# Kernel tuning notes

Hardware: AMD Instinct MI355X
Metric: run time of the kernel (lower is better)

The kernel has to match this reference:

```python
import jax, jax.numpy as jnp
import numpy as np

NUM_USERS = 600000
NUM_ITEMS = 400000
NUM_NODES = NUM_USERS + NUM_ITEMS
DIM = 64
NUM_EDGES = 8000000


def setup_inputs() -> dict:
    key = jax.random.key(0)
    k1, k2, k3, k4 = jax.random.split(key, 4)
    users_emb = jax.random.normal(k1, (NUM_USERS, DIM), dtype=jnp.float32)
    items_emb = jax.random.normal(k2, (NUM_ITEMS, DIM), dtype=jnp.float32)
    edge_index = jax.random.randint(k3, (2, NUM_EDGES), 0, NUM_NODES, dtype=jnp.int64)
    edge_values = jax.random.uniform(k4, (NUM_EDGES,), dtype=jnp.float32)
    return {
        "users_emb": users_emb,
        "items_emb": items_emb,
        "edge_index": edge_index,
        "edge_values": edge_values,
    }


def reference(users_emb, items_emb, edge_index, edge_values):
    # all_emb = cat([users_emb, items_emb])  -> [N, d]
    num_user = users_emb.shape[0]
    num_item = items_emb.shape[0]
    all_emb = jnp.concatenate([users_emb, items_emb], axis=0)
    # SpMM: out[r] = sum_{e: row[e]==r} val[e] * all_emb[col[e]]
    rows, cols = edge_index[0], edge_index[1]
    messages = all_emb[cols] * edge_values[:, None]  # [E, d] gather + scale
    out = jax.ops.segment_sum(messages, rows, num_segments=num_user + num_item)
    h_u2 = out[:num_user]
    h_i2 = out[num_user:]
    return (h_u2, h_i2)
```

## Files before the change

### kernel.cpp

```cpp
#include <hip/hip_runtime.h>

#define DIM 64
#define RPB 1024
#define RPB_SHIFT 10
#define NBMAX 1024
#define CHUNK 4096
#define EPT 16
#define CAPT 36
#define NPG 4
#define NPB 128
#define REC_CAP 1536

typedef unsigned long long u64;
typedef unsigned int u32;
typedef unsigned short u16;
typedef float f4v __attribute__((ext_vector_type(4)));
typedef _Float16 h4 __attribute__((ext_vector_type(4)));
typedef _Float16 h8 __attribute__((ext_vector_type(8)));

__global__ void detect_idx_width(const unsigned int* __restrict__ idx_words,
                                 int* __restrict__ flag) {
    __shared__ unsigned int s_or[256];
    unsigned int acc = 0;
    for (int i = threadIdx.x; i < 4096; i += blockDim.x)
        acc |= idx_words[2 * i + 1];
    s_or[threadIdx.x] = acc;
    __syncthreads();
    for (int s = 128; s > 0; s >>= 1) {
        if (threadIdx.x < s) s_or[threadIdx.x] |= s_or[threadIdx.x + s];
        __syncthreads();
    }
    if (threadIdx.x == 0) *flag = (s_or[0] == 0) ? 1 : 0;
}

__device__ __forceinline__ int load_idx(const void* ei, int use64, long long i) {
    return use64 ? (int)((const long long*)ei)[i] : ((const int*)ei)[i];
}

__global__ __launch_bounds__(256) void convert_emb(const f4v* __restrict__ u4,
                                                   const f4v* __restrict__ i4,
                                                   long long usz4, long long tot4,
                                                   h4* __restrict__ dst) {
    long long stride = (long long)gridDim.x * blockDim.x;
    for (long long idx = (long long)blockIdx.x * blockDim.x + threadIdx.x;
         idx < tot4; idx += stride) {
        const f4v* src = (idx < usz4) ? (u4 + idx) : (i4 + (idx - usz4));
        f4v f = __builtin_nontemporal_load(src);
        h4 o;
        o.x = (_Float16)f.x; o.y = (_Float16)f.y;
        o.z = (_Float16)f.z; o.w = (_Float16)f.w;
        __builtin_nontemporal_store(o, dst + idx);
    }
}

__global__ __launch_bounds__(256) void hist_coarse(const void* __restrict__ ei,
                                                   const int* __restrict__ flag,
                                                   int* __restrict__ counts,
                                                   int num_edges) {
    __shared__ int h[NBMAX];
    for (int b = threadIdx.x; b < NBMAX; b += 256) h[b] = 0;
    __syncthreads();
    int use64 = *flag;
    long long tid = (long long)blockIdx.x * 256 + threadIdx.x;
    long long stride = (long long)gridDim.x * 256;
    long long npairs = (long long)num_edges >> 1;
    if (use64) {
        const ulonglong2* p = (const ulonglong2*)ei;
        for (long long e = tid; e < npairs; e += stride) {
            ulonglong2 rr = p[e];
            atomicAdd(&h[(int)(u32)rr.x >> RPB_SHIFT], 1);
            atomicAdd(&h[(int)(u32)rr.y >> RPB_SHIFT], 1);
        }
    } else {
        const int2* p = (const int2*)ei;
        for (long long e = tid; e < npairs; e += stride) {
            int2 rr = p[e];
            atomicAdd(&h[rr.x >> RPB_SHIFT], 1);
            atomicAdd(&h[rr.y >> RPB_SHIFT], 1);
        }
    }
    if (tid == 0 && (num_edges & 1)) {
        int r = load_idx(ei, use64, num_edges - 1);
        atomicAdd(&h[r >> RPB_SHIFT], 1);
    }
    __syncthreads();
    for (int b = threadIdx.x; b < NBMAX; b += 256)
        if (h[b]) atomicAdd(&counts[b], h[b]);
}

__global__ __launch_bounds__(256) void scan_buckets(const int* __restrict__ counts,
                                                    int* __restrict__ offs,
                                                    int* __restrict__ gcursor,
                                                    int* __restrict__ offs2, int nbkt) {
    __shared__ int ps[256];
    int t = threadIdx.x;
    int4 h = ((const int4*)counts)[t];
    ps[t] = h.x + h.y + h.z + h.w;
    __syncthreads();
    for (int st = 1; st < 256; st <<= 1) {
        int add = (t >= st) ? ps[t - st] : 0;
        __syncthreads();
        ps[t] += add;
        __syncthreads();
    }
    int ep = (t > 0) ? ps[t - 1] : 0;
    int o0 = ep, o1 = o0 + h.x, o2 = o1 + h.y, o3 = o2 + h.z;
    offs[4*t] = o0; offs[4*t+1] = o1; offs[4*t+2] = o2; offs[4*t+3] = o3;
    gcursor[4*t] = o0; gcursor[4*t+1] = o1; gcursor[4*t+2] = o2; gcursor[4*t+3] = o3;
    if (t == 255) {
        offs[NBMAX] = ps[255];
        offs2[(long long)nbkt << RPB_SHIFT] = ps[255];
    }
}

__global__ __launch_bounds__(256) void bin_edges(const void* __restrict__ ei,
                                                 const float* __restrict__ vals,
                                                 const int* __restrict__ flag,
                                                 int* __restrict__ gcursor,
                                                 u64* __restrict__ recs,
                                                 int num_edges) {
    __shared__ u32 hist[NBMAX];
    __shared__ u32 scanL[NBMAX];
    __shared__ u32 gbase[NBMAX];
    __shared__ u32 ps[256];
    __shared__ u64 payload[CHUNK];
    __shared__ u16 bidv[CHUNK];

    int tid = threadIdx.x;
    long long base = (long long)blockIdx.x * CHUNK;
    int n = (int)min((long long)CHUNK, (long long)num_edges - base);
    int use64 = *flag;

    for (int b = tid; b < NBMAX; b += 256) hist[b] = 0;
    __syncthreads();

    int rows_[EPT]; int cols_[EPT]; float ws_[EPT];
    #pragma unroll
    for (int i = 0; i < EPT; ++i) {
        int j = tid + i * 256;
        rows_[i] = -1;
        if (j < n) {
            long long e = base + j;
            rows_[i] = load_idx(ei, use64, e);
            cols_[i] = load_idx(ei, use64, (long long)num_edges + e);
            ws_[i]   = vals[e];
            atomicAdd(&hist[rows_[i] >> RPB_SHIFT], 1u);
        }
    }
    __syncthreads();

    u32 h0 = hist[4*tid], h1 = hist[4*tid+1], h2 = hist[4*tid+2], h3 = hist[4*tid+3];
    ps[tid] = h0 + h1 + h2 + h3;
    __syncthreads();
    for (int st = 1; st < 256; st <<= 1) {
        u32 add = (tid >= st) ? ps[tid - st] : 0;
        __syncthreads();
        ps[tid] += add;
        __syncthreads();
    }
    u32 ep = (tid > 0) ? ps[tid - 1] : 0;
    scanL[4*tid]   = ep;
    scanL[4*tid+1] = ep + h0;
    scanL[4*tid+2] = ep + h0 + h1;
    scanL[4*tid+3] = ep + h0 + h1 + h2;
    __syncthreads();

    for (int b = tid; b < NBMAX; b += 256) {
        u32 c = hist[b];
        gbase[b] = c ? (u32)atomicAdd(&gcursor[b], (int)c) : 0u;
    }
    __syncthreads();
    for (int b = tid; b < NBMAX; b += 256) hist[b] = scanL[b];
    __syncthreads();

    #pragma unroll
    for (int i = 0; i < EPT; ++i) {
        if (rows_[i] >= 0) {
            int b = rows_[i] >> RPB_SHIFT;
            u32 pos = atomicAdd(&hist[b], 1u);
            u32 rl = (u32)(rows_[i] & (RPB - 1));
            payload[pos] = ((u64)__float_as_uint(ws_[i]) << 32) | (rl << 20) | (u32)cols_[i];
            bidv[pos] = (u16)b;
        }
    }
    __syncthreads();

    for (int j = tid; j < n; j += 256) {
        u64 rec = payload[j];
        int b = bidv[j];
        recs[gbase[b] + (u32)j - scanL[b]] = rec;
    }
}

__global__ __launch_bounds__(256, 2) void sort_bucket(const int* __restrict__ offs,
                                                      u64* __restrict__ recs,
                                                      int* __restrict__ offs2) {
    __shared__ u32 bins[RPB];
    __shared__ u32 ps[256];
    int b = blockIdx.x;
    int t = threadIdx.x;
    int beg = offs[b], end = offs[b + 1];
    int cnt = end - beg;
    int row0 = b << RPB_SHIFT;

    if (cnt > CAPT * 256) {
        for (int i = t; i < RPB; i += 256) offs2[row0 + i] = -(b + 1);
        return;
    }

    u64 r_[CAPT];
    #pragma unroll
    for (int k = 0; k < CAPT; ++k) {
        int j = t + k * 256;
        r_[k] = (j < cnt) ? recs[beg + j] : 0ull;
    }
    for (int i = t; i < RPB; i += 256) bins[i] = 0;
    __syncthreads();

    #pragma unroll
    for (int k = 0; k < CAPT; ++k) {
        int j = t + k * 256;
        if (j < cnt) atomicAdd(&bins[(u32)(r_[k] >> 20) & (RPB - 1)], 1u);
    }
    __syncthreads();

    u32 c0[4]; u32 s = 0;
    #pragma unroll
    for (int i = 0; i < 4; ++i) { c0[i] = bins[t * 4 + i]; s += c0[i]; }
    ps[t] = s;
    __syncthreads();
    for (int st = 1; st < 256; st <<= 1) {
        u32 add = (t >= st) ? ps[t - st] : 0;
        __syncthreads();
        ps[t] += add;
        __syncthreads();
    }
    u32 ex = (t > 0) ? ps[t - 1] : 0;
    #pragma unroll
    for (int i = 0; i < 4; ++i) {
        bins[t * 4 + i] = ex;
        offs2[row0 + t * 4 + i] = beg + (int)ex;
        ex += c0[i];
    }
    __syncthreads();

    #pragma unroll
    for (int k = 0; k < CAPT; ++k) {
        int j = t + k * 256;
        if (j < cnt) {
            u32 rl = (u32)(r_[k] >> 20) & (RPB - 1);
            u32 pos = atomicAdd(&bins[rl], 1u);
            recs[beg + pos] = r_[k];
        }
    }
}

#define ACC8(P0, P1, W, V) \
    P0.x += W * (float)V[0]; P0.y += W * (float)V[1]; \
    P0.z += W * (float)V[2]; P0.w += W * (float)V[3]; \
    P1.x += W * (float)V[4]; P1.y += W * (float)V[5]; \
    P1.z += W * (float)V[6]; P1.w += W * (float)V[7];

__global__ __launch_bounds__(256) void gather_nodes_h(const int* __restrict__ offs,
                                                      const int* __restrict__ offs2,
                                                      const u64* __restrict__ recs,
                                                      const h8* __restrict__ hemb8,
                                                      float* __restrict__ out,
                                                      int num_nodes) {
    __shared__ int s_offs[NPB + 1];
    __shared__ int s_bad;
    __shared__ u64 s_recs[REC_CAP];

    int tid = threadIdx.x;
    int l8  = tid & 7;
    int g   = tid >> 3;
    long long n0 = (long long)blockIdx.x * NPB;

    if (tid == 0) s_bad = 0;
    __syncthreads();
    if (tid <= NPB) {
        int v = offs2[n0 + tid];
        s_offs[tid] = v;
        if (v < 0) s_bad = 1;
    }
    __syncthreads();

    int rbeg = s_offs[0];
    int cnt  = s_offs[NPB] - rbeg;
    bool fast = (s_bad == 0) && ((u32)cnt <= (u32)REC_CAP);

    if (fast) {
        for (int j = tid; j < cnt; j += 256)
            s_recs[j] = __builtin_nontemporal_load(&recs[rbeg + j]);
    }
    __syncthreads();

    if (fast) {
        for (int nn = 0; nn < NPG; ++nn) {
            int ln = g * NPG + nn;
            int node = (int)n0 + ln;
            if (node >= num_nodes) break;
            int beg = s_offs[ln] - rbeg;
            int end = s_offs[ln + 1] - rbeg;

            float4 p0 = make_float4(0.f,0.f,0.f,0.f), p1 = make_float4(0.f,0.f,0.f,0.f);
            float4 q0 = make_float4(0.f,0.f,0.f,0.f), q1 = make_float4(0.f,0.f,0.f,0.f);

            int i = beg;
            for (; i + 8 <= end; i += 8) {
                u64 s0 = s_recs[i];     u64 s1 = s_recs[i + 1];
                u64 s2 = s_recs[i + 2]; u64 s3 = s_recs[i + 3];
                u64 s4 = s_recs[i + 4]; u64 s5 = s_recs[i + 5];
                u64 s6 = s_recs[i + 6]; u64 s7 = s_recs[i + 7];
                h8 v0 = hemb8[(((u32)s0 & 0xFFFFFu) << 3) + l8];
                h8 v1 = hemb8[(((u32)s1 & 0xFFFFFu) << 3) + l8];
                h8 v2 = hemb8[(((u32)s2 & 0xFFFFFu) << 3) + l8];
                h8 v3 = hemb8[(((u32)s3 & 0xFFFFFu) << 3) + l8];
                h8 v4 = hemb8[(((u32)s4 & 0xFFFFFu) << 3) + l8];
                h8 v5 = hemb8[(((u32)s5 & 0xFFFFFu) << 3) + l8];
                h8 v6 = hemb8[(((u32)s6 & 0xFFFFFu) << 3) + l8];
                h8 v7 = hemb8[(((u32)s7 & 0xFFFFFu) << 3) + l8];
                float w0 = __uint_as_float((u32)(s0 >> 32));
                float w1 = __uint_as_float((u32)(s1 >> 32));
                float w2 = __uint_as_float((u32)(s2 >> 32));
                float w3 = __uint_as_float((u32)(s3 >> 32));
                float w4 = __uint_as_float((u32)(s4 >> 32));
                float w5 = __uint_as_float((u32)(s5 >> 32));
                float w6 = __uint_as_float((u32)(s6 >> 32));
                float w7 = __uint_as_float((u32)(s7 >> 32));
                ACC8(p0, p1, w0, v0); ACC8(q0, q1, w1, v1);
                ACC8(p0, p1, w2, v2); ACC8(q0, q1, w3, v3);
                ACC8(p0, p1, w4, v4); ACC8(q0, q1, w5, v5);
                ACC8(p0, p1, w6, v6); ACC8(q0, q1, w7, v7);
            }
            if (i < end) {
                int last = end - 1;
                int e1 = min(i + 1, last), e2 = min(i + 2, last);
                int e3 = min(i + 3, last), e4 = min(i + 4, last);
                int e5 = min(i + 5, last), e6 = min(i + 6, last);
                u64 s0 = s_recs[i];  u64 s1 = s_recs[e1];
                u64 s2 = s_recs[e2]; u64 s3 = s_recs[e3];
                u64 s4 = s_recs[e4]; u64 s5 = s_recs[e5];
                u64 s6 = s_recs[e6];
                h8 v0 = hemb8[(((u32)s0 & 0xFFFFFu) << 3) + l8];
                h8 v1 = hemb8[(((u32)s1 & 0xFFFFFu) << 3) + l8];
                h8 v2 = hemb8[(((u32)s2 & 0xFFFFFu) << 3) + l8];
                h8 v3 = hemb8[(((u32)s3 & 0xFFFFFu) << 3) + l8];
                h8 v4 = hemb8[(((u32)s4 & 0xFFFFFu) << 3) + l8];
                h8 v5 = hemb8[(((u32)s5 & 0xFFFFFu) << 3) + l8];
                h8 v6 = hemb8[(((u32)s6 & 0xFFFFFu) << 3) + l8];
                float w0 = __uint_as_float((u32)(s0 >> 32));
                float w1 = (i + 1 < end) ? __uint_as_float((u32)(s1 >> 32)) : 0.f;
                float w2 = (i + 2 < end) ? __uint_as_float((u32)(s2 >> 32)) : 0.f;
                float w3 = (i + 3 < end) ? __uint_as_float((u32)(s3 >> 32)) : 0.f;
                float w4 = (i + 4 < end) ? __uint_as_float((u32)(s4 >> 32)) : 0.f;
                float w5 = (i + 5 < end) ? __uint_as_float((u32)(s5 >> 32)) : 0.f;
                float w6 = (i + 6 < end) ? __uint_as_float((u32)(s6 >> 32)) : 0.f;
                ACC8(p0, p1, w0, v0); ACC8(q0, q1, w1, v1);
                ACC8(p0, p1, w2, v2); ACC8(q0, q1, w3, v3);
                ACC8(p0, p1, w4, v4); ACC8(q0, q1, w5, v5);
                ACC8(p0, p1, w6, v6);
            }

            p0.x += q0.x; p0.y += q0.y; p0.z += q0.z; p0.w += q0.w;
            p1.x += q1.x; p1.y += q1.y; p1.z += q1.z; p1.w += q1.w;
            f4v o0; o0.x = p0.x; o0.y = p0.y; o0.z = p0.z; o0.w = p0.w;
            f4v o1; o1.x = p1.x; o1.y = p1.y; o1.z = p1.z; o1.w = p1.w;
            f4v* dst = (f4v*)out + ((long long)node << 4) + (l8 << 1);
            __builtin_nontemporal_store(o0, dst);
            __builtin_nontemporal_store(o1, dst + 1);
        }
    } else {
        for (int nn = 0; nn < NPG; ++nn) {
            int ln = g * NPG + nn;
            int node = (int)n0 + ln;
            if (node >= num_nodes) break;
            int beg = s_offs[ln];
            int end = s_offs[ln + 1];
            if (beg < 0) { int b = node >> RPB_SHIFT; beg = offs[b]; end = offs[b + 1]; }
            else if (end < 0) { end = offs[(node >> RPB_SHIFT) + 1]; }
            u32 rl = (u32)(node & (RPB - 1));

            float4 p0 = make_float4(0.f,0.f,0.f,0.f), p1 = make_float4(0.f,0.f,0.f,0.f);
            float4 q0 = make_float4(0.f,0.f,0.f,0.f), q1 = make_float4(0.f,0.f,0.f,0.f);
            int last = end - 1;
            u32 rm = RPB - 1;
            for (int i = beg; i < end; i += 4) {
                int e1 = min(i + 1, last), e2 = min(i + 2, last), e3 = min(i + 3, last);
                u64 s0 = recs[i];  u64 s1 = recs[e1];
                u64 s2 = recs[e2]; u64 s3 = recs[e3];
                h8 v0 = hemb8[(((u32)s0 & 0xFFFFFu) << 3) + l8];
                h8 v1 = hemb8[(((u32)s1 & 0xFFFFFu) << 3) + l8];
                h8 v2 = hemb8[(((u32)s2 & 0xFFFFFu) << 3) + l8];
                h8 v3 = hemb8[(((u32)s3 & 0xFFFFFu) << 3) + l8];
                float w0 = ((((u32)(s0 >> 20)) & rm) == rl)
                           ? __uint_as_float((u32)(s0 >> 32)) : 0.f;
                float w1 = (((((u32)(s1 >> 20)) & rm) == rl) & (i + 1 < end))
                           ? __uint_as_float((u32)(s1 >> 32)) : 0.f;
                float w2 = (((((u32)(s2 >> 20)) & rm) == rl) & (i + 2 < end))
                           ? __uint_as_float((u32)(s2 >> 32)) : 0.f;
                float w3 = (((((u32)(s3 >> 20)) & rm) == rl) & (i + 3 < end))
                           ? __uint_as_float((u32)(s3 >> 32)) : 0.f;
                ACC8(p0, p1, w0, v0); ACC8(q0, q1, w1, v1);
                ACC8(p0, p1, w2, v2); ACC8(q0, q1, w3, v3);
            }
            p0.x += q0.x; p0.y += q0.y; p0.z += q0.z; p0.w += q0.w;
            p1.x += q1.x; p1.y += q1.y; p1.z += q1.z; p1.w += q1.w;
            f4v o0; o0.x = p0.x; o0.y = p0.y; o0.z = p0.z; o0.w = p0.w;
            f4v o1; o1.x = p1.x; o1.y = p1.y; o1.z = p1.z; o1.w = p1.w;
            f4v* dst = (f4v*)out + ((long long)node << 4) + (l8 << 1);
            __builtin_nontemporal_store(o0, dst);
            __builtin_nontemporal_store(o1, dst + 1);
        }
    }
}

__device__ __forceinline__ void gstep(u64 s, u32 rl,
                                      const float* __restrict__ users,
                                      const float* __restrict__ items_m,
                                      int num_users, int l16, float4& a) {
    int c = (int)(s & 0xFFFFFu);
    float w = __uint_as_float((u32)(s >> 32));
    w = (((u32)(s >> 20) & (RPB - 1)) == rl) ? w : 0.f;
    const float* p = ((c < num_users) ? users : items_m) + ((u32)c << 6);
    float4 m = reinterpret_cast<const float4*>(p)[l16];
    a.x += w * m.x; a.y += w * m.y; a.z += w * m.z; a.w += w * m.w;
}

__global__ __launch_bounds__(256) void gather_nodes(const int* __restrict__ offs,
                                                    const int* __restrict__ offs2,
                                                    const u64* __restrict__ recs,
                                                    const float* __restrict__ users,
                                                    const float* __restrict__ items_m,
                                                    float* __restrict__ out,
                                                    int num_users, int num_nodes) {
    int node = blockIdx.x * (blockDim.x >> 6) + (threadIdx.x >> 6);
    int lane = threadIdx.x & 63;
    if (node >= num_nodes) return;
    int q   = lane >> 4;
    int l16 = lane & 15;

    int beg = offs2[node];
    int end = offs2[node + 1];
    if (beg < 0) { int b = node >> RPB_SHIFT; beg = offs[b]; end = offs[b + 1]; }
    else if (end < 0) { end = offs[(node >> RPB_SHIFT) + 1]; }
    u32 rl = (u32)(node & (RPB - 1));

    float4 a0 = make_float4(0.f, 0.f, 0.f, 0.f);
    float4 a1 = make_float4(0.f, 0.f, 0.f, 0.f);

    int i = beg + q;
    for (; i + 4 < end; i += 8) {
        u64 s0 = recs[i];
        u64 s1 = recs[i + 4];
        gstep(s0, rl, users, items_m, num_users, l16, a0);
        gstep(s1, rl, users, items_m, num_users, l16, a1);
    }
    if (i < end) {
        u64 s0 = recs[i];
        gstep(s0, rl, users, items_m, num_users, l16, a0);
    }
    a0.x += a1.x; a0.y += a1.y; a0.z += a1.z; a0.w += a1.w;

    for (int msk = 16; msk <= 32; msk <<= 1) {
        a0.x += __shfl_xor(a0.x, msk, 64);
        a0.y += __shfl_xor(a0.y, msk, 64);
        a0.z += __shfl_xor(a0.z, msk, 64);
        a0.w += __shfl_xor(a0.w, msk, 64);
    }
    if (q == 0)
        reinterpret_cast<float4*>(out)[(long long)node * 16 + l16] = a0;
}

__global__ __launch_bounds__(256) void scatter_edges(const void* __restrict__ edge_index,
                                                     const float* __restrict__ vals,
                                                     const float* __restrict__ users,
                                                     const float* __restrict__ items,
                                                     float* __restrict__ out,
                                                     const int* __restrict__ idx64_flag,
                                                     int num_users, int num_edges) {
    long long gid = (long long)blockIdx.x * blockDim.x + threadIdx.x;
    long long e = gid >> 4;
    int lane = (int)(gid & 15);
    if (e >= num_edges) return;
    int use64 = *idx64_flag;
    int r = load_idx(edge_index, use64, e);
    int c = load_idx(edge_index, use64, (long long)num_edges + e);
    float w = vals[e];
    const float* src = (c < num_users)
        ? (users + (long long)c * DIM)
        : (items + (long long)(c - num_users) * DIM);
    float4 m = reinterpret_cast<const float4*>(src)[lane];
    float* dst = out + (long long)r * DIM + lane * 4;
    unsafeAtomicAdd(dst + 0, m.x * w);
    unsafeAtomicAdd(dst + 1, m.y * w);
    unsafeAtomicAdd(dst + 2, m.z * w);
    unsafeAtomicAdd(dst + 3, m.w * w);
}

extern "C" void kernel_launch(void* const* d_in, const int* in_sizes, int n_in,
                              void* d_out, int out_size, void* d_ws, size_t ws_size,
                              hipStream_t stream) {
    const float* users = (const float*)d_in[0];
    const float* items = (const float*)d_in[1];
    const void*  eidx  = d_in[2];
    const float* vals  = (const float*)d_in[3];
    float* out = (float*)d_out;

    int num_users = in_sizes[0] / DIM;
    int num_items = in_sizes[1] / DIM;
    int num_nodes = num_users + num_items;
    int num_edges = in_sizes[3];
    int nbkt = (num_nodes + RPB - 1) >> RPB_SHIFT;

    size_t off = 0;
    auto alloc = [&](size_t bytes) { size_t p = off; off = (off + bytes + 255) & ~(size_t)255; return p; };
    size_t o_flag   = alloc(4);
    size_t o_counts = alloc((size_t)NBMAX * 4);
    size_t o_offs   = alloc(((size_t)NBMAX + 1) * 4);
    size_t o_gcur   = alloc((size_t)NBMAX * 4);
    size_t o_recs   = alloc((size_t)num_edges * 8 + 64);
    size_t o_offs2  = alloc((((size_t)nbkt << RPB_SHIFT) + 1) * 4);
    size_t need_base = off;
    size_t o_hemb   = alloc((size_t)num_nodes * DIM * 2);
    size_t need_f16 = off;

    char* ws = (char*)d_ws;
    int* flag = (int*)(ws + o_flag);

    detect_idx_width<<<1, 256, 0, stream>>>((const unsigned int*)eidx, flag);

    if (ws_size < need_base || nbkt > NBMAX || num_nodes > (1 << 20)) {
        hipMemsetAsync(d_out, 0, (size_t)out_size * sizeof(float), stream);
        long long total_threads = (long long)num_edges * 16;
        long long grid = (total_threads + 255) / 256;
        scatter_edges<<<(int)grid, 256, 0, stream>>>(
            eidx, vals, users, items, out, flag, num_users, num_edges);
        return;
    }

    int* counts  = (int*)(ws + o_counts);
    int* offs    = (int*)(ws + o_offs);
    int* gcursor = (int*)(ws + o_gcur);
    u64* recs    = (u64*)(ws + o_recs);
    int* offs2   = (int*)(ws + o_offs2);
    h4*  hemb4   = (h4*)(ws + o_hemb);

    bool use_f16 = (ws_size >= need_f16) && ((DIM % 8) == 0);

    hipMemsetAsync(counts, 0, (size_t)NBMAX * 4, stream);

    if (use_f16) {
        long long usz4 = (long long)num_users * DIM / 4;
        long long tot4 = (long long)num_nodes * DIM / 4;
        convert_emb<<<2048, 256, 0, stream>>>((const f4v*)users, (const f4v*)items,
                                              usz4, tot4, hemb4);
    }

    hist_coarse<<<1024, 256, 0, stream>>>(eidx, flag, counts, num_edges);
    scan_buckets<<<1, 256, 0, stream>>>(counts, offs, gcursor, offs2, nbkt);

    int bin_grid = (num_edges + CHUNK - 1) / CHUNK;
    bin_edges<<<bin_grid, 256, 0, stream>>>(eidx, vals, flag, gcursor, recs, num_edges);

    sort_bucket<<<nbkt, 256, 0, stream>>>(offs, recs, offs2);

    if (use_f16) {
        int gg = (num_nodes + NPB - 1) / NPB;
        gather_nodes_h<<<gg, 256, 0, stream>>>(offs, offs2, recs,
                                               (const h8*)hemb4, out, num_nodes);
    } else {
        int gg = (num_nodes + 3) / 4;
        const float* items_m = items - (size_t)num_users * DIM;
        gather_nodes<<<gg, 256, 0, stream>>>(offs, offs2, recs, users, items_m, out,
                                             num_users, num_nodes);
    }
}
```

Before: 466.5 us.

## Use wave-shuffle block scans, nontemporal index loads, larger binning chunks

Replaces the shared-memory Hillis-Steele block scans in scan_buckets, bin_edges and sort_bucket with a wave-level shuffle scan plus a small cross-wave combine, which removes many barriers. Raises the binning chunk to 6144 edges and 24 per thread with launch bounds of two blocks per CU, and shrinks the hist_coarse grid. Index and value loads become nontemporal, and the fp16 embedding store becomes a normal store so it can stay in cache for the gather. The larger chunk raises register and LDS use in bin_edges, which may cut occupancy.

```diff
diff --git a/kernel.cpp b/kernel.cpp
--- a/kernel.cpp
+++ b/kernel.cpp
@@ -4,8 +4,8 @@
 #define RPB 1024
 #define RPB_SHIFT 10
 #define NBMAX 1024
-#define CHUNK 4096
-#define EPT 16
+#define CHUNK 6144
+#define EPT 24
 #define CAPT 36
 #define NPG 4
 #define NPB 128
@@ -35,6 +35,28 @@
 
 __device__ __forceinline__ int load_idx(const void* ei, int use64, long long i) {
     return use64 ? (int)((const long long*)ei)[i] : ((const int*)ei)[i];
+}
+
+__device__ __forceinline__ int load_idx_nt(const void* ei, int use64, long long i) {
+    return use64 ? (int)__builtin_nontemporal_load(&((const long long*)ei)[i])
+                 : __builtin_nontemporal_load(&((const int*)ei)[i]);
+}
+
+__device__ __forceinline__ u32 quad_scan_ex(u32 qs, u32* wtot, int tid, u32* total_out) {
+    u32 inc = qs;
+    #pragma unroll
+    for (int d = 1; d < 64; d <<= 1) {
+        u32 v = __shfl_up(inc, d, 64);
+        if ((tid & 63) >= d) inc += v;
+    }
+    if ((tid & 63) == 63) wtot[tid >> 6] = inc;
+    __syncthreads();
+    int w = tid >> 6;
+    u32 woff = 0;
+    #pragma unroll
+    for (int k = 0; k < 3; ++k) woff += (k < w) ? wtot[k] : 0;
+    if (total_out) *total_out = wtot[0] + wtot[1] + wtot[2] + wtot[3];
+    return woff + inc - qs;
 }
 
 __global__ __launch_bounds__(256) void convert_emb(const f4v* __restrict__ u4,
@@ -49,7 +71,7 @@
         h4 o;
         o.x = (_Float16)f.x; o.y = (_Float16)f.y;
         o.z = (_Float16)f.z; o.w = (_Float16)f.w;
-        __builtin_nontemporal_store(o, dst + idx);
+        dst[idx] = o;
     }
 }
 
@@ -64,19 +86,19 @@
     long long tid = (long long)blockIdx.x * 256 + threadIdx.x;
     long long stride = (long long)gridDim.x * 256;
     long long npairs = (long long)num_edges >> 1;
+    const u64* p = (const u64*)ei;
     if (use64) {
-        const ulonglong2* p = (const ulonglong2*)ei;
         for (long long e = tid; e < npairs; e += stride) {
-            ulonglong2 rr = p[e];
-            atomicAdd(&h[(int)(u32)rr.x >> RPB_SHIFT], 1);
-            atomicAdd(&h[(int)(u32)rr.y >> RPB_SHIFT], 1);
+            u64 a = __builtin_nontemporal_load(&p[2 * e]);
+            u64 b = __builtin_nontemporal_load(&p[2 * e + 1]);
+            atomicAdd(&h[(int)(u32)a >> RPB_SHIFT], 1);
+            atomicAdd(&h[(int)(u32)b >> RPB_SHIFT], 1);
         }
     } else {
-        const int2* p = (const int2*)ei;
         for (long long e = tid; e < npairs; e += stride) {
-            int2 rr = p[e];
-            atomicAdd(&h[rr.x >> RPB_SHIFT], 1);
-            atomicAdd(&h[rr.y >> RPB_SHIFT], 1);
+            u64 v = __builtin_nontemporal_load(&p[e]);
+            atomicAdd(&h[(int)(u32)v >> RPB_SHIFT], 1);
+            atomicAdd(&h[(int)(u32)(v >> 32) >> RPB_SHIFT], 1);
         }
     }
     if (tid == 0 && (num_edges & 1)) {
@@ -92,37 +114,31 @@
                                                     int* __restrict__ offs,
                                                     int* __restrict__ gcursor,
                                                     int* __restrict__ offs2, int nbkt) {
-    __shared__ int ps[256];
+    __shared__ u32 wtot[4];
     int t = threadIdx.x;
     int4 h = ((const int4*)counts)[t];
-    ps[t] = h.x + h.y + h.z + h.w;
-    __syncthreads();
-    for (int st = 1; st < 256; st <<= 1) {
-        int add = (t >= st) ? ps[t - st] : 0;
-        __syncthreads();
-        ps[t] += add;
-        __syncthreads();
-    }
-    int ep = (t > 0) ? ps[t - 1] : 0;
-    int o0 = ep, o1 = o0 + h.x, o2 = o1 + h.y, o3 = o2 + h.z;
+    u32 qs = (u32)(h.x + h.y + h.z + h.w);
+    u32 total;
+    u32 ex = quad_scan_ex(qs, wtot, t, &total);
+    int o0 = (int)ex, o1 = o0 + h.x, o2 = o1 + h.y, o3 = o2 + h.z;
     offs[4*t] = o0; offs[4*t+1] = o1; offs[4*t+2] = o2; offs[4*t+3] = o3;
     gcursor[4*t] = o0; gcursor[4*t+1] = o1; gcursor[4*t+2] = o2; gcursor[4*t+3] = o3;
     if (t == 255) {
-        offs[NBMAX] = ps[255];
-        offs2[(long long)nbkt << RPB_SHIFT] = ps[255];
-    }
-}
-
-__global__ __launch_bounds__(256) void bin_edges(const void* __restrict__ ei,
-                                                 const float* __restrict__ vals,
-                                                 const int* __restrict__ flag,
-                                                 int* __restrict__ gcursor,
-                                                 u64* __restrict__ recs,
-                                                 int num_edges) {
+        offs[NBMAX] = (int)total;
+        offs2[(long long)nbkt << RPB_SHIFT] = (int)total;
+    }
+}
+
+__global__ __launch_bounds__(256, 2) void bin_edges(const void* __restrict__ ei,
+                                                    const float* __restrict__ vals,
+                                                    const int* __restrict__ flag,
+                                                    int* __restrict__ gcursor,
+                                                    u64* __restrict__ recs,
+                                                    int num_edges) {
     __shared__ u32 hist[NBMAX];
     __shared__ u32 scanL[NBMAX];
     __shared__ u32 gbase[NBMAX];
-    __shared__ u32 ps[256];
+    __shared__ u32 wtot[4];
     __shared__ u64 payload[CHUNK];
     __shared__ u16 bidv[CHUNK];
 
@@ -141,28 +157,20 @@
         rows_[i] = -1;
         if (j < n) {
             long long e = base + j;
-            rows_[i] = load_idx(ei, use64, e);
-            cols_[i] = load_idx(ei, use64, (long long)num_edges + e);
-            ws_[i]   = vals[e];
+            rows_[i] = load_idx_nt(ei, use64, e);
+            cols_[i] = load_idx_nt(ei, use64, (long long)num_edges + e);
+            ws_[i]   = __builtin_nontemporal_load(&vals[e]);
             atomicAdd(&hist[rows_[i] >> RPB_SHIFT], 1u);
         }
     }
     __syncthreads();
 
     u32 h0 = hist[4*tid], h1 = hist[4*tid+1], h2 = hist[4*tid+2], h3 = hist[4*tid+3];
-    ps[tid] = h0 + h1 + h2 + h3;
-    __syncthreads();
-    for (int st = 1; st < 256; st <<= 1) {
-        u32 add = (tid >= st) ? ps[tid - st] : 0;
-        __syncthreads();
-        ps[tid] += add;
-        __syncthreads();
-    }
-    u32 ep = (tid > 0) ? ps[tid - 1] : 0;
-    scanL[4*tid]   = ep;
-    scanL[4*tid+1] = ep + h0;
-    scanL[4*tid+2] = ep + h0 + h1;
-    scanL[4*tid+3] = ep + h0 + h1 + h2;
+    u32 ex = quad_scan_ex(h0 + h1 + h2 + h3, wtot, tid, nullptr);
+    scanL[4*tid]   = ex;
+    scanL[4*tid+1] = ex + h0;
+    scanL[4*tid+2] = ex + h0 + h1;
+    scanL[4*tid+3] = ex + h0 + h1 + h2;
     __syncthreads();
 
     for (int b = tid; b < NBMAX; b += 256) {
@@ -196,7 +204,7 @@
                                                       u64* __restrict__ recs,
                                                       int* __restrict__ offs2) {
     __shared__ u32 bins[RPB];
-    __shared__ u32 ps[256];
+    __shared__ u32 wtot[4];
     int b = blockIdx.x;
     int t = threadIdx.x;
     int beg = offs[b], end = offs[b + 1];
@@ -227,15 +235,7 @@
     u32 c0[4]; u32 s = 0;
     #pragma unroll
     for (int i = 0; i < 4; ++i) { c0[i] = bins[t * 4 + i]; s += c0[i]; }
-    ps[t] = s;
-    __syncthreads();
-    for (int st = 1; st < 256; st <<= 1) {
-        u32 add = (t >= st) ? ps[t - st] : 0;
-        __syncthreads();
-        ps[t] += add;
-        __syncthreads();
-    }
-    u32 ex = (t > 0) ? ps[t - 1] : 0;
+    u32 ex = quad_scan_ex(s, wtot, t, nullptr);
     #pragma unroll
     for (int i = 0; i < 4; ++i) {
         bins[t * 4 + i] = ex;
@@ -557,7 +557,7 @@
                                               usz4, tot4, hemb4);
     }
 
-    hist_coarse<<<1024, 256, 0, stream>>>(eidx, flag, counts, num_edges);
+    hist_coarse<<<768, 256, 0, stream>>>(eidx, flag, counts, num_edges);
     scan_buckets<<<1, 256, 0, stream>>>(counts, offs, gcursor, offs2, nbkt);
 
     int bin_grid = (num_edges + CHUNK - 1) / CHUNK;
```

Measured after the change: 473.1 us. No clear change (+1.4%).
